# Kernel tuning notes

Measured on AMD Instinct MI355X. Metric: run time of the kernel, lower is better.

The kernel has to match this reference:

```python
import jax, jax.numpy as jnp
import numpy as np

NUM_GROUPS = 32
EPS = 1e-5


def _conv(x, w, b, pad):
    # x: [B,C,H,W], w: [O,I,kh,kw]
    y = jax.lax.conv_general_dilated(
        x, w, window_strides=(1, 1), padding=[(pad, pad), (pad, pad)],
        dimension_numbers=('NCHW', 'OIHW', 'NCHW'))
    return y + b[None, :, None, None]


def _group_norm(x, gamma, beta):
    B, C, H, W = x.shape
    g = x.reshape(B, NUM_GROUPS, C // NUM_GROUPS, H, W)
    mu = g.mean(axis=(2, 3, 4), keepdims=True)
    var = g.var(axis=(2, 3, 4), keepdims=True)
    g = (g - mu) * jax.lax.rsqrt(var + EPS)
    x = g.reshape(B, C, H, W)
    return x * gamma[None, :, None, None] + beta[None, :, None, None]


def setup_inputs() -> dict:
    key = jax.random.key(0)
    ks = jax.random.split(key, 8)
    B, C, H, W = 8, 384, 64, 64
    s1 = 1.0 / np.sqrt(C)          # 1x1 conv fan-in
    s3 = 1.0 / np.sqrt(C * 9)      # 3x3 conv fan-in
    return {
        'x': jax.random.normal(ks[0], (B, C, H, W), dtype=jnp.float32),
        'gamma': jnp.ones((C,), dtype=jnp.float32),
        'beta': jnp.zeros((C,), dtype=jnp.float32),
        'wq': jax.random.normal(ks[1], (C, C, 1, 1), dtype=jnp.float32) * s1,
        'bq': jnp.zeros((C,), dtype=jnp.float32),
        'wk': jax.random.normal(ks[2], (C, C, 3, 3), dtype=jnp.float32) * s3,
        'bk': jnp.zeros((C,), dtype=jnp.float32),
        'wv': jax.random.normal(ks[3], (C, C, 1, 1), dtype=jnp.float32) * s1,
        'bv': jnp.zeros((C,), dtype=jnp.float32),
        'wf': jax.random.normal(ks[4], (C, C, 1, 1), dtype=jnp.float32) * s1,
        'bf': jnp.zeros((C,), dtype=jnp.float32),
        'k': 512,
    }


def reference(x, gamma, beta, wq, bq, wk, bk, wv, bv, wf, bf, k):
    B, C, H, W = x.shape
    xn = _group_norm(x, gamma, beta)
    q = _conv(xn, wq, bq, 0)
    kk = _conv(xn, wk, bk, 1)
    v = _conv(xn, wv, bv, 0)
    # frequency-domain correlation: elementwise product of 2D spectra
    Fq = jnp.fft.fft2(q)
    Fk = jnp.fft.fft2(kk)
    A = jnp.fft.ifft2(Fq * Fk).real          # [B,C,H,W]
    # per-(batch,channel) spatial top-k sparsification
    A_flat = A.reshape(B, C, H * W)
    topv, _ = jax.lax.top_k(A_flat, k)
    thresh = topv[..., -1:]                   # k-th largest value
    masked = jnp.where(A_flat >= thresh, A_flat, -jnp.inf)
    Fw = jax.nn.softmax(masked, axis=-1).reshape(B, C, H, W)
    F4 = v * Fw                               # weighted values
    res = _conv(F4, wf, bf, 0)
    return xn * res
```

## Files before the change

kernel.cpp:

```cpp
#include <hip/hip_runtime.h>
#include <hip/hip_fp16.h>
#include <math.h>

#define CCH  384
#define BATCH 8
#define HWN  4096
#define NG   32
#define CPG  12
#define KSEL 512
#define FFTP 65
#define LP   40

typedef short v8s  __attribute__((ext_vector_type(8)));
typedef float v16f __attribute__((ext_vector_type(16)));

#define MFMA_B16(A_,B_,C_) __builtin_amdgcn_mfma_f32_32x32x16_bf16((A_),(B_),(C_),0,0,0)

__device__ __forceinline__ unsigned br6(unsigned i) {
  return ((i&1u)<<5)|((i&2u)<<3)|((i&4u)<<1)|((i&8u)>>1)|((i&16u)>>3)|((i&32u)>>5);
}
__device__ __forceinline__ unsigned f2key(float f) {
  unsigned u = __float_as_uint(f);
  return (u & 0x80000000u) ? ~u : (u | 0x80000000u);
}
__device__ __forceinline__ float wave_max(float v) {
#pragma unroll
  for (int o = 32; o > 0; o >>= 1) v = fmaxf(v, __shfl_down(v, o, 64));
  return v;
}
__device__ __forceinline__ float wave_sum(float v) {
#pragma unroll
  for (int o = 32; o > 0; o >>= 1) v += __shfl_down(v, o, 64);
  return v;
}
__device__ __forceinline__ unsigned short bf16_rne(float f) {
  unsigned u = __float_as_uint(f);
  return (unsigned short)((u + 0x7fffu + ((u >> 16) & 1u)) >> 16);
}
__device__ __forceinline__ float bf2f(unsigned short h) {
  return __uint_as_float(((unsigned)h) << 16);
}

__global__ __launch_bounds__(256) void stats_kernel(const float* __restrict__ x,
                                                    float2* __restrict__ gs) {
  int b = blockIdx.x >> 5, g = blockIdx.x & 31;
  size_t base = ((size_t)b * CCH + (size_t)g * CPG) * HWN;
  const float4* xp = (const float4*)(x + base);
  int tid = threadIdx.x;
  const int N4 = CPG * HWN / 4;
  float s = 0.f, ss = 0.f;
  for (int i = tid; i < N4; i += 256) {
    float4 v = xp[i];
    s  += (v.x + v.y) + (v.z + v.w);
    ss += (v.x*v.x + v.y*v.y) + (v.z*v.z + v.w*v.w);
  }
  s = wave_sum(s); ss = wave_sum(ss);
  __shared__ float sb[4], qb[4];
  if ((tid & 63) == 0) { sb[tid >> 6] = s; qb[tid >> 6] = ss; }
  __syncthreads();
  if (tid == 0) {
    float S = sb[0]+sb[1]+sb[2]+sb[3], Q = qb[0]+qb[1]+qb[2]+qb[3];
    float inv = 1.0f / (float)(CPG * HWN);
    float mu = S * inv;
    float var = Q * inv - mu * mu;
    gs[blockIdx.x] = make_float2(mu, rsqrtf(var + 1e-5f));
  }
}

__global__ __launch_bounds__(256) void pack_split_k(const float* __restrict__ w,
    unsigned short* __restrict__ hi, unsigned short* __restrict__ lo, int n) {
  int i = blockIdx.x * 256 + threadIdx.x;
  if (i >= n) return;
  float f = w[i];
  unsigned short h = bf16_rne(f);
  hi[i] = h;
  lo[i] = bf16_rne(f - bf2f(h));
}
__global__ __launch_bounds__(256) void pack9_k(const float* __restrict__ w,
    unsigned short* __restrict__ hi, unsigned short* __restrict__ lo) {
  int i = blockIdx.x * 256 + threadIdx.x;
  int r = blockIdx.y;
  float f = w[(size_t)i * 9 + r];
  unsigned short h = bf16_rne(f);
  size_t o = (size_t)r * 147456 + i;
  hi[o] = h;
  lo[o] = bf16_rne(f - bf2f(h));
}

template<int FUSE, int SPLIT>
__global__ __launch_bounds__(256) void trans_kernel(const float* __restrict__ in,
    const float2* __restrict__ gs, const float* __restrict__ gamma,
    const float* __restrict__ beta,
    unsigned short* __restrict__ oh, unsigned short* __restrict__ ol) {
  __shared__ float ts[64][65];
  int tid = threadIdx.x;
  int b = blockIdx.z, c0 = blockIdx.y * 64, p0 = blockIdx.x * 64;
#pragma unroll
  for (int i = 0; i < 4; ++i) {
    int idx = tid + (i << 8);
    int row = idx >> 4, col = (idx & 15) << 2;
    float4 v = *(const float4*)&in[((size_t)b*CCH + c0 + row)*HWN + p0 + col];
    if (FUSE) {
      int c = c0 + row;
      float2 st = gs[(b << 5) + c / CPG];
      float a = gamma[c] * st.y, bb = beta[c] - st.x * a;
      v.x = v.x*a+bb; v.y = v.y*a+bb; v.z = v.z*a+bb; v.w = v.w*a+bb;
    }
    ts[row][col] = v.x; ts[row][col+1] = v.y; ts[row][col+2] = v.z; ts[row][col+3] = v.w;
  }
  __syncthreads();
#pragma unroll
  for (int i = 0; i < 2; ++i) {
    int idx = tid + (i << 8);
    int p = idx >> 3, cgp = (idx & 7) << 3;
    unsigned short h8[8] __attribute__((aligned(16)));
    unsigned short l8[8] __attribute__((aligned(16)));
#pragma unroll
    for (int j = 0; j < 8; ++j) {
      float f = ts[cgp + j][p];
      unsigned short hb = bf16_rne(f);
      h8[j] = hb;
      if (SPLIT) l8[j] = bf16_rne(f - bf2f(hb));
    }
    size_t o = ((size_t)b*HWN + p0 + p)*CCH + c0 + cgp;
    *(uint4*)&oh[o] = *(const uint4*)h8;
    if (SPLIT) *(uint4*)&ol[o] = *(const uint4*)l8;
  }
}

template<int TAPS, int OUT>
__global__ __launch_bounds__(256, 3) void mm_kernel(
    const unsigned short* __restrict__ Ahg, const unsigned short* __restrict__ Alg,
    const float* __restrict__ bias,
    const unsigned short* __restrict__ Bhg, const unsigned short* __restrict__ Blg,
    const unsigned short* __restrict__ xnTh, const unsigned short* __restrict__ xnTl,
    void* __restrict__ Yv) {
  __shared__ unsigned short Ah_s[128*LP], Al_s[128*LP], Bh_s[128*LP], Bl_s[128*LP];
  int tid = threadIdx.x;
  int b = blockIdx.z, m0 = blockIdx.y * 128, n0 = blockIdx.x * 128;
  int y0 = blockIdx.x * 2;
  int u0row = tid >> 2, cg = tid & 3;
  int lds0 = u0row * LP + cg * 8, lds1 = lds0 + 64 * LP;
  size_t aoff0 = (size_t)(m0 + u0row) * CCH + cg * 8;
  int lane = tid & 63, wm = tid >> 7, wn = (tid >> 6) & 1;
  int lm = lane & 31, lh = lane >> 5;
  int arow = (wm * 64 + lm) * LP, brow = (wn * 64 + lm) * LP;

  v16f acc[2][2];
#pragma unroll
  for (int t = 0; t < 2; ++t)
#pragma unroll
    for (int s = 0; s < 2; ++s)
#pragma unroll
      for (int g = 0; g < 16; ++g) acc[t][s][g] = 0.f;

  const int NS = TAPS * 12;
  uint4 ra0h, ra0l, ra1h, ra1l, rb0h, rb0l, rb1h, rb1l;

  auto issue = [&](int s) {
    int r  = (TAPS == 9) ? (s / 12) : 0;
    int c0 = (s - r * 12) * 32;
    const unsigned short* Arh = Ahg + (size_t)r * CCH * CCH + aoff0 + c0;
    const unsigned short* Arl = Alg + (size_t)r * CCH * CCH + aoff0 + c0;
    ra0h = *(const uint4*)Arh;
    ra0l = *(const uint4*)Arl;
    ra1h = *(const uint4*)(Arh + 64 * CCH);
    ra1l = *(const uint4*)(Arl + 64 * CCH);
    int dy = (TAPS == 9) ? r / 3 - 1 : 0;
    int dx = (TAPS == 9) ? r % 3 - 1 : 0;
    int px = u0row + dx;
    int py0 = y0 + dy, py1 = py0 + 1;
    bool okx = (unsigned)px < 64u;
    bool ok0 = okx && ((unsigned)py0 < 64u);
    bool ok1 = okx && ((unsigned)py1 < 64u);
    size_t boff0 = ((size_t)b * HWN + py0 * 64 + px) * CCH + cg * 8 + c0;
    size_t boff1 = ((size_t)b * HWN + py1 * 64 + px) * CCH + cg * 8 + c0;
    uint4 zf; zf.x = zf.y = zf.z = zf.w = 0u;
    rb0h = ok0 ? *(const uint4*)(Bhg + boff0) : zf;
    rb0l = ok0 ? *(const uint4*)(Blg + boff0) : zf;
    rb1h = ok1 ? *(const uint4*)(Bhg + boff1) : zf;
    rb1l = ok1 ? *(const uint4*)(Blg + boff1) : zf;
  };

  issue(0);
  for (int s = 0; s < NS; ++s) {
    __syncthreads();
    *(uint4*)&Ah_s[lds0] = ra0h; *(uint4*)&Al_s[lds0] = ra0l;
    *(uint4*)&Ah_s[lds1] = ra1h; *(uint4*)&Al_s[lds1] = ra1l;
    *(uint4*)&Bh_s[lds0] = rb0h; *(uint4*)&Bl_s[lds0] = rb0l;
    *(uint4*)&Bh_s[lds1] = rb1h; *(uint4*)&Bl_s[lds1] = rb1l;
    __syncthreads();
    if (s + 1 < NS) issue(s + 1);
#pragma unroll
    for (int h = 0; h < 2; ++h) {
      int co = h * 16 + lh * 8;
      v8s a0h = *(const v8s*)&Ah_s[arow + co];
      v8s a1h = *(const v8s*)&Ah_s[arow + 32*LP + co];
      v8s a0l = *(const v8s*)&Al_s[arow + co];
      v8s a1l = *(const v8s*)&Al_s[arow + 32*LP + co];
      v8s b0h = *(const v8s*)&Bh_s[brow + co];
      v8s b1h = *(const v8s*)&Bh_s[brow + 32*LP + co];
      v8s b0l = *(const v8s*)&Bl_s[brow + co];
      v8s b1l = *(const v8s*)&Bl_s[brow + 32*LP + co];
      acc[0][0] = MFMA_B16(a0h, b0h, acc[0][0]);
      acc[0][0] = MFMA_B16(a0h, b0l, acc[0][0]);
      acc[0][0] = MFMA_B16(a0l, b0h, acc[0][0]);
      acc[0][1] = MFMA_B16(a0h, b1h, acc[0][1]);
      acc[0][1] = MFMA_B16(a0h, b1l, acc[0][1]);
      acc[0][1] = MFMA_B16(a0l, b1h, acc[0][1]);
      acc[1][0] = MFMA_B16(a1h, b0h, acc[1][0]);
      acc[1][0] = MFMA_B16(a1h, b0l, acc[1][0]);
      acc[1][0] = MFMA_B16(a1l, b0h, acc[1][0]);
      acc[1][1] = MFMA_B16(a1h, b1h, acc[1][1]);
      acc[1][1] = MFMA_B16(a1h, b1l, acc[1][1]);
      acc[1][1] = MFMA_B16(a1l, b1h, acc[1][1]);
    }
  }
#pragma unroll
  for (int t = 0; t < 2; ++t) {
    int mb = m0 + wm * 64 + t * 32;
#pragma unroll
    for (int s = 0; s < 2; ++s) {
      int n = n0 + wn * 64 + s * 32 + lm;
#pragma unroll
      for (int g = 0; g < 16; ++g) {
        int m = mb + (g & 3) + ((g >> 2) << 3) + (lh << 2);
        float val = acc[t][s][g] + bias[m];
        size_t oidx = ((size_t)b * CCH + m) * HWN + n;
        if (OUT == 0) {
          ((float*)Yv)[oidx] = val;
        } else if (OUT == 1) {
          ((__half*)Yv)[oidx] = __float2half(val);
        } else {
          size_t tix = ((size_t)b * HWN + n) * CCH + m;
          float xnv = bf2f(xnTh[tix]) + bf2f(xnTl[tix]);
          ((float*)Yv)[oidx] = val * xnv;
        }
      }
    }
  }
}

__device__ __forceinline__ void fft4_pass(float* zr, float* zi,
    const float* twr, const float* twi, int tid, int axis, float ds) {
#pragma unroll
  for (int s = 0; s < 3; ++s) {
    const int h = 1 << (2 * s);
#pragma unroll
    for (int tt = 0; tt < 4; ++tt) {
      int t = tid + (tt << 8);
      int line = t >> 4, bf = t & 15;
      int j  = bf & (h - 1);
      int i0 = ((bf >> (2 * s)) << (2 * s + 2)) + j;
      int e1 = j << (5 - 2 * s);
      int e2 = j << (4 - 2 * s);
      float w1r = twr[e1], w1i = ds * twi[e1];
      float w2r = twr[e2], w2i = ds * twi[e2];
      int A0, st;
      if (axis == 0) { A0 = line * FFTP + i0; st = h; }
      else           { A0 = i0 * FFTP + line; st = h * FFTP; }
      int A1 = A0 + st, A2 = A1 + st, A3 = A2 + st;
      float x0r = zr[A0], x0i = zi[A0];
      float x1r = zr[A1], x1i = zi[A1];
      float x2r = zr[A2], x2i = zi[A2];
      float x3r = zr[A3], x3i = zi[A3];
      float t1r = x1r*w1r - x1i*w1i, t1i = x1r*w1i + x1i*w1r;
      float t3r = x3r*w1r - x3i*w1i, t3i = x3r*w1i + x3i*w1r;
      float u0r = x0r + t1r, u0i = x0i + t1i;
      float u1r = x0r - t1r, u1i = x0i - t1i;
      float u2r = x2r + t3r, u2i = x2i + t3i;
      float u3r = x2r - t3r, u3i = x2i - t3i;
      float c2r = u2r*w2r - u2i*w2i, c2i = u2r*w2i + u2i*w2r;
      float c3r = u3r*w2r - u3i*w2i, c3i = u3r*w2i + u3i*w2r;
      zr[A0] = u0r + c2r;      zi[A0] = u0i + c2i;
      zr[A2] = u0r - c2r;      zi[A2] = u0i - c2i;
      zr[A1] = u1r + ds*c3i;   zi[A1] = u1i - ds*c3r;
      zr[A3] = u1r - ds*c3i;   zi[A3] = u1i + ds*c3r;
    }
    __syncthreads();
  }
}

__global__ __launch_bounds__(256) void fft_topk_kernel(
    const float* q, const float* __restrict__ kkb,
    const __half* __restrict__ v, float* F4) {
  __shared__ float zr[64 * FFTP], zi[64 * FFTP];
  __shared__ float twr[32], twi[32];
  __shared__ unsigned hist[256];
  __shared__ unsigned su2[2];
  __shared__ unsigned wtot[4];
  __shared__ float sred[5];
  int tid = threadIdx.x;
  int lane = tid & 63, w = tid >> 6;
  size_t base = (size_t)blockIdx.x * HWN;
  for (int i = tid; i < HWN; i += 256) {
    int y = i >> 6, x = i & 63;
    int slot = br6(y) * FFTP + br6(x);
    zr[slot] = q[base + i];
    zi[slot] = kkb[base + i];
  }
  if (tid < 32) {
    float ang = (float)tid * 0.0981747704246810387f;
    twr[tid] = cosf(ang);
    twi[tid] = -sinf(ang);
  }
  __syncthreads();
  fft4_pass(zr, zi, twr, twi, tid, 0, 1.f);
  fft4_pass(zr, zi, twr, twi, tid, 1, 1.f);
  float prr[16], pir[16];
#pragma unroll
  for (int c = 0; c < 16; c++) {
    int i = tid + (c << 8);
    int ky = i >> 6, kx = i & 63;
    float sr = zr[ky * FFTP + kx], si = zi[ky * FFTP + kx];
    int kyn = (64 - ky) & 63, kxn = (64 - kx) & 63;
    float nr = zr[kyn * FFTP + kxn], ni = zi[kyn * FFTP + kxn];
    float fqr = 0.5f * (sr + nr), fqi = 0.5f * (si - ni);
    float fkr = 0.5f * (si + ni), fki = 0.5f * (nr - sr);
    prr[c] = fqr * fkr - fqi * fki;
    pir[c] = fqr * fki + fqi * fkr;
  }
  __syncthreads();
#pragma unroll
  for (int c = 0; c < 16; c++) {
    int i = tid + (c << 8);
    int ky = i >> 6, kx = i & 63;
    int slot = br6(ky) * FFTP + br6(kx);
    zr[slot] = prr[c];
    zi[slot] = pir[c];
  }
  __syncthreads();
  fft4_pass(zr, zi, twr, twi, tid, 0, -1.f);
  fft4_pass(zr, zi, twr, twi, tid, 1, -1.f);
  const float scale = 1.0f / 4096.0f;
  float a[16];
  unsigned key[16];
  float mx = -3.0e38f;
#pragma unroll
  for (int c = 0; c < 16; c++) {
    int i = tid + (c << 8);
    a[c] = zr[(i >> 6) * FFTP + (i & 63)] * scale;
    key[c] = f2key(a[c]);
    mx = fmaxf(mx, a[c]);
  }
  mx = wave_max(mx);
  if (lane == 0) sred[w] = mx;
  __syncthreads();
  if (tid == 0) sred[4] = fmaxf(fmaxf(sred[0], sred[1]), fmaxf(sred[2], sred[3]));
  __syncthreads();
  float am = sred[4];
  unsigned prefix = 0; int kr = KSEL;
  for (int pass = 0; pass < 4; pass++) {
    int shift = 24 - (pass << 3);
    hist[tid] = 0;
    __syncthreads();
#pragma unroll
    for (int c = 0; c < 16; c++) {
      unsigned u = key[c];
      if (((u ^ prefix) >> shift) <= 0xFFu)
        atomicAdd(&hist[(u >> shift) & 255u], 1u);
    }
    __syncthreads();
    unsigned xv = hist[tid];
#pragma unroll
    for (int o = 1; o < 64; o <<= 1) {
      unsigned t2 = __shfl_down(xv, o, 64);
      if (lane + o < 64) xv += t2;
    }
    if (lane == 0) wtot[w] = xv;
    __syncthreads();
    for (int ww = w + 1; ww < 4; ++ww) xv += wtot[ww];
    hist[tid] = xv;
    __syncthreads();
    unsigned sv = xv;
    unsigned svn = (tid < 255) ? hist[tid + 1] : 0u;
    if (sv >= (unsigned)kr && svn < (unsigned)kr) { su2[0] = (unsigned)tid; su2[1] = svn; }
    __syncthreads();
    prefix |= su2[0] << shift;
    kr -= (int)su2[1];
  }
  unsigned thr = prefix;
  float lsum = 0.f;
#pragma unroll
  for (int c = 0; c < 16; c++)
    if (key[c] >= thr) lsum += expf(a[c] - am);
  lsum = wave_sum(lsum);
  if (lane == 0) sred[w] = lsum;
  __syncthreads();
  if (tid == 0) sred[4] = 1.0f / (sred[0] + sred[1] + sred[2] + sred[3]);
  __syncthreads();
  float inv = sred[4];
#pragma unroll
  for (int c = 0; c < 16; c++) {
    int i = tid + (c << 8);
    float wgt = (key[c] >= thr) ? expf(a[c] - am) * inv : 0.f;
    F4[base + i] = __half2float(v[base + i]) * wgt;
  }
}

extern "C" void kernel_launch(void* const* d_in, const int* in_sizes, int n_in,
                              void* d_out, int out_size, void* d_ws, size_t ws_size,
                              hipStream_t stream) {
  const float* x     = (const float*)d_in[0];
  const float* gamma = (const float*)d_in[1];
  const float* beta  = (const float*)d_in[2];
  const float* wq    = (const float*)d_in[3];
  const float* bq    = (const float*)d_in[4];
  const float* wk    = (const float*)d_in[5];
  const float* bk    = (const float*)d_in[6];
  const float* wv    = (const float*)d_in[7];
  const float* bv    = (const float*)d_in[8];
  const float* wf    = (const float*)d_in[9];
  const float* bf    = (const float*)d_in[10];

  const size_t NEL = (size_t)BATCH * CCH * HWN;
  const size_t WSZ = (size_t)CCH * CCH;

  unsigned short* xnTh = (unsigned short*)d_ws;
  unsigned short* xnTl = xnTh + NEL;
  float*  qC  = (float*)(xnTl + NEL);
  float*  kD  = qC + NEL;
  __half* vE  = (__half*)(kD + NEL);
  unsigned short* W = (unsigned short*)(vE + NEL);
  unsigned short* Wqh = W;
  unsigned short* Wql = Wqh + WSZ;
  unsigned short* Wvh = Wql + WSZ;
  unsigned short* Wvl = Wvh + WSZ;
  unsigned short* Wfh = Wvl + WSZ;
  unsigned short* Wfl = Wfh + WSZ;
  unsigned short* Wkh = Wfl + WSZ;
  unsigned short* Wkl = Wkh + 9 * WSZ;
  float2* gs = (float2*)(Wkl + 9 * WSZ);
  unsigned short* F4Th = (unsigned short*)kD;
  unsigned short* F4Tl = F4Th + NEL;

  pack_split_k<<<dim3(576), dim3(256), 0, stream>>>(wq, Wqh, Wql, (int)WSZ);
  pack_split_k<<<dim3(576), dim3(256), 0, stream>>>(wv, Wvh, Wvl, (int)WSZ);
  pack_split_k<<<dim3(576), dim3(256), 0, stream>>>(wf, Wfh, Wfl, (int)WSZ);
  pack9_k<<<dim3(576, 9), dim3(256), 0, stream>>>(wk, Wkh, Wkl);
  stats_kernel<<<dim3(BATCH * NG), dim3(256), 0, stream>>>(x, gs);
  trans_kernel<1, 1><<<dim3(64, 6, BATCH), dim3(256), 0, stream>>>(
      x, gs, gamma, beta, xnTh, xnTl);

  dim3 gm(32, 3, BATCH);
  mm_kernel<1, 0><<<gm, dim3(256), 0, stream>>>(Wqh, Wql, bq, xnTh, xnTl,
                                                nullptr, nullptr, qC);
  mm_kernel<9, 0><<<gm, dim3(256), 0, stream>>>(Wkh, Wkl, bk, xnTh, xnTl,
                                                nullptr, nullptr, kD);
  mm_kernel<1, 1><<<gm, dim3(256), 0, stream>>>(Wvh, Wvl, bv, xnTh, xnTl,
                                                nullptr, nullptr, vE);

  fft_topk_kernel<<<dim3(BATCH * CCH), dim3(256), 0, stream>>>(qC, kD, vE, qC);

  trans_kernel<0, 1><<<dim3(64, 6, BATCH), dim3(256), 0, stream>>>(
      qC, nullptr, nullptr, nullptr, F4Th, F4Tl);

  mm_kernel<1, 2><<<gm, dim3(256), 0, stream>>>(Wfh, Wfl, bf, F4Th, F4Tl,
                                                xnTh, xnTl, d_out);
}
```

Before: 674.8 us.

## Prepack weights in MFMA fragment order, load A directly to registers, double-buffer B

Weight packing kernels now write bf16 hi/lo weights in a per-lane MFMA fragment layout. The GEMM kernel then loads A operands straight from global memory into registers and drops the A shared-memory tiles. B tiles are double-buffered in LDS, so each k-step needs one barrier instead of two, and the next A and B loads are issued while the current MFMAs run. This cuts LDS traffic and synchronisation but raises register pressure, which may hurt occupancy under the 3-blocks launch bound.

```diff
diff --git a/kernel.cpp b/kernel.cpp
--- a/kernel.cpp
+++ b/kernel.cpp
@@ -16,6 +16,9 @@
 
 #define MFMA_B16(A_,B_,C_) __builtin_amdgcn_mfma_f32_32x32x16_bf16((A_),(B_),(C_),0,0,0)
 
+__device__ __forceinline__ v8s as_v8s(uint4 u) {
+  union { uint4 u4; v8s v; } c; c.u4 = u; return c.v;
+}
 __device__ __forceinline__ unsigned br6(unsigned i) {
   return ((i&1u)<<5)|((i&2u)<<3)|((i&4u)<<1)|((i&8u)>>1)|((i&16u)>>3)|((i&32u)>>5);
 }
@@ -72,17 +75,28 @@
   int i = blockIdx.x * 256 + threadIdx.x;
   if (i >= n) return;
   float f = w[i];
+  int m = i / 384, ci = i - m * 384;
+  int kc = ci >> 4, tt = ci & 15;
+  int mb = m >> 5, lm2 = m & 31;
+  int l = ((tt >> 3) << 5) | lm2;
+  int j = tt & 7;
+  size_t o = (((size_t)kc * 12 + mb) << 9) + ((size_t)l << 3) + j;
   unsigned short h = bf16_rne(f);
-  hi[i] = h;
-  lo[i] = bf16_rne(f - bf2f(h));
+  hi[o] = h;
+  lo[o] = bf16_rne(f - bf2f(h));
 }
 __global__ __launch_bounds__(256) void pack9_k(const float* __restrict__ w,
     unsigned short* __restrict__ hi, unsigned short* __restrict__ lo) {
   int i = blockIdx.x * 256 + threadIdx.x;
   int r = blockIdx.y;
   float f = w[(size_t)i * 9 + r];
+  int m = i / 384, ci = i - m * 384;
+  int kc = ci >> 4, tt = ci & 15;
+  int mb = m >> 5, lm2 = m & 31;
+  int l = ((tt >> 3) << 5) | lm2;
+  int j = tt & 7;
+  size_t o = (((size_t)(r * 24 + kc) * 12 + mb) << 9) + ((size_t)l << 3) + j;
   unsigned short h = bf16_rne(f);
-  size_t o = (size_t)r * 147456 + i;
   hi[o] = h;
   lo[o] = bf16_rne(f - bf2f(h));
 }
@@ -135,16 +149,17 @@
     const unsigned short* __restrict__ Bhg, const unsigned short* __restrict__ Blg,
     const unsigned short* __restrict__ xnTh, const unsigned short* __restrict__ xnTl,
     void* __restrict__ Yv) {
-  __shared__ unsigned short Ah_s[128*LP], Al_s[128*LP], Bh_s[128*LP], Bl_s[128*LP];
+  __shared__ unsigned short Bh_s[2][128*LP], Bl_s[2][128*LP];
   int tid = threadIdx.x;
   int b = blockIdx.z, m0 = blockIdx.y * 128, n0 = blockIdx.x * 128;
   int y0 = blockIdx.x * 2;
   int u0row = tid >> 2, cg = tid & 3;
   int lds0 = u0row * LP + cg * 8, lds1 = lds0 + 64 * LP;
-  size_t aoff0 = (size_t)(m0 + u0row) * CCH + cg * 8;
   int lane = tid & 63, wm = tid >> 7, wn = (tid >> 6) & 1;
   int lm = lane & 31, lh = lane >> 5;
-  int arow = (wm * 64 + lm) * LP, brow = (wn * 64 + lm) * LP;
+  int brow = (wn * 64 + lm) * LP;
+  int mbb = blockIdx.y * 4 + wm * 2;
+  int laneoff = lane << 3;
 
   v16f acc[2][2];
 #pragma unroll
@@ -155,17 +170,13 @@
       for (int g = 0; g < 16; ++g) acc[t][s][g] = 0.f;
 
   const int NS = TAPS * 12;
-  uint4 ra0h, ra0l, ra1h, ra1l, rb0h, rb0l, rb1h, rb1l;
-
-  auto issue = [&](int s) {
+  uint4 rb0h, rb0l, rb1h, rb1l;
+  uint4 rA0h_h0, rA0l_h0, rA1h_h0, rA1l_h0;
+  uint4 rA0h_h1, rA0l_h1, rA1h_h1, rA1l_h1;
+
+  auto issueB = [&](int s) {
     int r  = (TAPS == 9) ? (s / 12) : 0;
     int c0 = (s - r * 12) * 32;
-    const unsigned short* Arh = Ahg + (size_t)r * CCH * CCH + aoff0 + c0;
-    const unsigned short* Arl = Alg + (size_t)r * CCH * CCH + aoff0 + c0;
-    ra0h = *(const uint4*)Arh;
-    ra0l = *(const uint4*)Arl;
-    ra1h = *(const uint4*)(Arh + 64 * CCH);
-    ra1l = *(const uint4*)(Arl + 64 * CCH);
     int dy = (TAPS == 9) ? r / 3 - 1 : 0;
     int dx = (TAPS == 9) ? r % 3 - 1 : 0;
     int px = u0row + dx;
@@ -181,27 +192,46 @@
     rb1h = ok1 ? *(const uint4*)(Bhg + boff1) : zf;
     rb1l = ok1 ? *(const uint4*)(Blg + boff1) : zf;
   };
-
-  issue(0);
+  auto loadA0 = [&](int s) {
+    int fragcol;
+    if (TAPS == 9) { int r = s / 12; fragcol = r * 24 + (s - r * 12) * 2; }
+    else fragcol = s * 2;
+    size_t off = (((size_t)fragcol * 12 + mbb) << 9) + laneoff;
+    rA0h_h0 = *(const uint4*)(Ahg + off);
+    rA0l_h0 = *(const uint4*)(Alg + off);
+    rA1h_h0 = *(const uint4*)(Ahg + off + 512);
+    rA1l_h0 = *(const uint4*)(Alg + off + 512);
+  };
+  auto loadA1 = [&](int s) {
+    int fragcol;
+    if (TAPS == 9) { int r = s / 12; fragcol = r * 24 + (s - r * 12) * 2 + 1; }
+    else fragcol = s * 2 + 1;
+    size_t off = (((size_t)fragcol * 12 + mbb) << 9) + laneoff;
+    rA0h_h1 = *(const uint4*)(Ahg + off);
+    rA0l_h1 = *(const uint4*)(Alg + off);
+    rA1h_h1 = *(const uint4*)(Ahg + off + 512);
+    rA1l_h1 = *(const uint4*)(Alg + off + 512);
+  };
+
+  issueB(0);
+  loadA0(0); loadA1(0);
+  *(uint4*)&Bh_s[0][lds0] = rb0h; *(uint4*)&Bl_s[0][lds0] = rb0l;
+  *(uint4*)&Bh_s[0][lds1] = rb1h; *(uint4*)&Bl_s[0][lds1] = rb1l;
+  issueB(1);
+  __syncthreads();
+
   for (int s = 0; s < NS; ++s) {
-    __syncthreads();
-    *(uint4*)&Ah_s[lds0] = ra0h; *(uint4*)&Al_s[lds0] = ra0l;
-    *(uint4*)&Ah_s[lds1] = ra1h; *(uint4*)&Al_s[lds1] = ra1l;
-    *(uint4*)&Bh_s[lds0] = rb0h; *(uint4*)&Bl_s[lds0] = rb0l;
-    *(uint4*)&Bh_s[lds1] = rb1h; *(uint4*)&Bl_s[lds1] = rb1l;
-    __syncthreads();
-    if (s + 1 < NS) issue(s + 1);
-#pragma unroll
-    for (int h = 0; h < 2; ++h) {
-      int co = h * 16 + lh * 8;
-      v8s a0h = *(const v8s*)&Ah_s[arow + co];
-      v8s a1h = *(const v8s*)&Ah_s[arow + 32*LP + co];
-      v8s a0l = *(const v8s*)&Al_s[arow + co];
-      v8s a1l = *(const v8s*)&Al_s[arow + 32*LP + co];
-      v8s b0h = *(const v8s*)&Bh_s[brow + co];
-      v8s b1h = *(const v8s*)&Bh_s[brow + 32*LP + co];
-      v8s b0l = *(const v8s*)&Bl_s[brow + co];
-      v8s b1l = *(const v8s*)&Bl_s[brow + 32*LP + co];
+    const int cur = s & 1;
+    const unsigned short* Bh = &Bh_s[cur][0];
+    const unsigned short* Bl = &Bl_s[cur][0];
+    {
+      int co = lh << 3;
+      v8s b0h = *(const v8s*)&Bh[brow + co];
+      v8s b0l = *(const v8s*)&Bl[brow + co];
+      v8s b1h = *(const v8s*)&Bh[brow + 32*LP + co];
+      v8s b1l = *(const v8s*)&Bl[brow + 32*LP + co];
+      v8s a0h = as_v8s(rA0h_h0), a0l = as_v8s(rA0l_h0);
+      v8s a1h = as_v8s(rA1h_h0), a1l = as_v8s(rA1l_h0);
       acc[0][0] = MFMA_B16(a0h, b0h, acc[0][0]);
       acc[0][0] = MFMA_B16(a0h, b0l, acc[0][0]);
       acc[0][0] = MFMA_B16(a0l, b0h, acc[0][0]);
@@ -214,6 +244,36 @@
       acc[1][1] = MFMA_B16(a1h, b1h, acc[1][1]);
       acc[1][1] = MFMA_B16(a1h, b1l, acc[1][1]);
       acc[1][1] = MFMA_B16(a1l, b1h, acc[1][1]);
+    }
+    if (s + 1 < NS) loadA0(s + 1);
+    {
+      int co = 16 + (lh << 3);
+      v8s b0h = *(const v8s*)&Bh[brow + co];
+      v8s b0l = *(const v8s*)&Bl[brow + co];
+      v8s b1h = *(const v8s*)&Bh[brow + 32*LP + co];
+      v8s b1l = *(const v8s*)&Bl[brow + 32*LP + co];
+      v8s a0h = as_v8s(rA0h_h1), a0l = as_v8s(rA0l_h1);
+      v8s a1h = as_v8s(rA1h_h1), a1l = as_v8s(rA1l_h1);
+      acc[0][0] = MFMA_B16(a0h, b0h, acc[0][0]);
+      acc[0][0] = MFMA_B16(a0h, b0l, acc[0][0]);
+      acc[0][0] = MFMA_B16(a0l, b0h, acc[0][0]);
+      acc[0][1] = MFMA_B16(a0h, b1h, acc[0][1]);
+      acc[0][1] = MFMA_B16(a0h, b1l, acc[0][1]);
+      acc[0][1] = MFMA_B16(a0l, b1h, acc[0][1]);
+      acc[1][0] = MFMA_B16(a1h, b0h, acc[1][0]);
+      acc[1][0] = MFMA_B16(a1h, b0l, acc[1][0]);
+      acc[1][0] = MFMA_B16(a1l, b0h, acc[1][0]);
+      acc[1][1] = MFMA_B16(a1h, b1h, acc[1][1]);
+      acc[1][1] = MFMA_B16(a1h, b1l, acc[1][1]);
+      acc[1][1] = MFMA_B16(a1l, b1h, acc[1][1]);
+    }
+    if (s + 1 < NS) {
+      loadA1(s + 1);
+      int nxt = cur ^ 1;
+      *(uint4*)&Bh_s[nxt][lds0] = rb0h; *(uint4*)&Bl_s[nxt][lds0] = rb0l;
+      *(uint4*)&Bh_s[nxt][lds1] = rb1h; *(uint4*)&Bl_s[nxt][lds1] = rb1l;
+      if (s + 2 < NS) issueB(s + 2);
+      __syncthreads();
     }
   }
 #pragma unroll
```

New measurement: 705.1 us. 4.5% more time.
